# Kernel optimization log

Measured on AMD Instinct MI355X. Metric: run time of the kernel, lower is better.

## Reference

```python
import jax, jax.numpy as jnp
import numpy as np


def _gather_corner(flat_feats, iz, iy, ix, H, W, B, F, Hg, Wg):
    # flat_feats: [B, F, D*H*W]; iz/iy/ix: [B, Hg, Wg] int32 (already clamped)
    lin = (iz * H + iy) * W + ix                      # [B, Hg, Wg]
    lin = jnp.broadcast_to(lin.reshape(B, 1, Hg * Wg), (B, F, Hg * Wg))
    return jnp.take_along_axis(flat_feats, lin, axis=2).reshape(B, F, Hg, Wg)


def setup_inputs() -> dict:
    key = jax.random.key(0)
    k1, k2 = jax.random.split(key)
    input_feats = jax.random.normal(k1, (4, 8, 128, 128, 128), dtype=jnp.float32)
    sampling_grid = jax.random.normal(k2, (4, 512, 512, 3), dtype=jnp.float32)
    return {"input_feats": input_feats, "sampling_grid": sampling_grid}


def reference(input_feats, sampling_grid):
    B, F, D, H, W = input_feats.shape
    Hg, Wg = sampling_grid.shape[1], sampling_grid.shape[2]

    # map grid from [-1,1] to voxel coordinates [0, dim-1]
    g = jnp.clip(sampling_grid, -1.0, 1.0)
    scale = jnp.array([W - 1.0, H - 1.0, D - 1.0], dtype=sampling_grid.dtype)
    g = (g + 1.0) * 0.5 * scale                      # [B, Hg, Wg, 3] in x,y,z order
    x, y, z = g[..., 0], g[..., 1], g[..., 2]

    x0 = jnp.floor(x); y0 = jnp.floor(y); z0 = jnp.floor(z)
    u = (x - x0)[:, None]                            # [B,1,Hg,Wg]
    v = (y - y0)[:, None]
    w = (z - z0)[:, None]

    # nearest grid_sample with align_corners=True on integer coords == clamped index
    def clampi(a, hi):
        return jnp.clip(a, 0, hi).astype(jnp.int32)

    ix0 = clampi(x0, W - 1); ix1 = clampi(x0 + 1.0, W - 1)
    iy0 = clampi(y0, H - 1); iy1 = clampi(y0 + 1.0, H - 1)
    iz0 = clampi(z0, D - 1); iz1 = clampi(z0 + 1.0, D - 1)

    flat = input_feats.reshape(B, F, D * H * W)
    gc = lambda iz, iy, ix: _gather_corner(flat, iz, iy, ix, H, W, B, F, Hg, Wg)

    c000 = gc(iz0, iy0, ix0); c001 = gc(iz1, iy0, ix0)
    c010 = gc(iz0, iy1, ix0); c011 = gc(iz1, iy1, ix0)
    c100 = gc(iz0, iy0, ix1); c101 = gc(iz1, iy0, ix1)
    c110 = gc(iz0, iy1, ix1); c111 = gc(iz1, iy1, ix1)

    out = ((1 - u) * (1 - v) * (1 - w) * c000 + (1 - u) * (1 - v) * w * c001
           + (1 - u) * v * (1 - w) * c010 + (1 - u) * v * w * c011
           + u * (1 - v) * (1 - w) * c100 + u * (1 - v) * w * c101
           + u * v * (1 - w) * c110 + u * v * w * c111)
    return out  # [B, F, Hg, Wg]
```

## Files before the change

### kernel.cpp

```cpp
#include <hip/hip_runtime.h>
#include <hip/hip_fp16.h>


#define NB 4
#define NF 8
#define ND 128
#define NH 128
#define NW 128
#define HG 512
#define WG 512

typedef float        __attribute__((ext_vector_type(4))) f32x4;
typedef unsigned int __attribute__((ext_vector_type(4))) u32x4;

__global__ __launch_bounds__(256) void transform_kernel(
    const float* __restrict__ feats, __half* __restrict__ T)
{
    const size_t S = (size_t)ND * NH * NW;
    size_t tid = (size_t)blockIdx.x * blockDim.x + threadIdx.x;
    size_t b  = tid / (S / 4);
    size_t s4 = (tid - b * (S / 4)) * 4;

    const float* fb = feats + b * NF * S;
    __half* tb = T + (b * S + s4) * NF;

    f32x4 vals[NF];
#pragma unroll
    for (int f = 0; f < NF; ++f)
        vals[f] = __builtin_nontemporal_load(
            (const f32x4*)(fb + (size_t)f * S + s4));

#pragma unroll
    for (int i = 0; i < 4; ++i) {
        u32x4 hv;
#pragma unroll
        for (int f = 0; f < 4; ++f) {
            __half2 h = __floats2half2_rn(vals[2 * f][i], vals[2 * f + 1][i]);
            hv[f] = *(const unsigned*)&h;
        }
        *(u32x4*)(tb + (size_t)i * NF) = hv;
    }
}

__device__ __forceinline__ void pair_accum(
    const u32x4& lov, const u32x4& hiv, bool hi,
    float wr, float um, float u, float acc[NF])
{
    u32x4 c0 = hi ? hiv : lov;
    const u32x4& c1 = hiv;
#pragma unroll
    for (int j = 0; j < 4; ++j) {
        unsigned u0 = c0[j], u1 = c1[j];
        float2 f0 = __half22float2(*(const __half2*)&u0);
        float2 f1 = __half22float2(*(const __half2*)&u1);
        acc[2 * j]     = fmaf(wr, fmaf(u, f1.x, um * f0.x), acc[2 * j]);
        acc[2 * j + 1] = fmaf(wr, fmaf(u, f1.y, um * f0.y), acc[2 * j + 1]);
    }
}

__global__ __launch_bounds__(256) void trilerp_half_kernel(
    const __half* __restrict__ T,
    const float* __restrict__ grid,
    float* __restrict__ out)
{
    const int P = HG * WG;
    int idx = blockIdx.x * blockDim.x + threadIdx.x;
    int b = idx >> 18;
    int p = idx & (P - 1);

    const float* g = grid + (size_t)idx * 3;
    float x = __builtin_nontemporal_load(g + 0);
    float y = __builtin_nontemporal_load(g + 1);
    float z = __builtin_nontemporal_load(g + 2);

    x = fminf(fmaxf(x, -1.0f), 1.0f);
    y = fminf(fmaxf(y, -1.0f), 1.0f);
    z = fminf(fmaxf(z, -1.0f), 1.0f);
    x = (x + 1.0f) * 0.5f * (float)(NW - 1);
    y = (y + 1.0f) * 0.5f * (float)(NH - 1);
    z = (z + 1.0f) * 0.5f * (float)(ND - 1);

    float xf = floorf(x), yf = floorf(y), zf = floorf(z);
    float u = x - xf, v = y - yf, w = z - zf;
    float um = 1.0f - u, vm = 1.0f - v, wm = 1.0f - w;

    int ix0 = min(max((int)xf, 0), NW - 1);
    int iy0 = min(max((int)yf, 0), NH - 1);
    int iy1 = min(iy0 + 1, NH - 1);
    int iz0 = min(max((int)zf, 0), ND - 1);
    int iz1 = min(iz0 + 1, ND - 1);

    int xb = min(ix0, NW - 2);
    bool hi = (ix0 != xb);

    const __half* tb = T + (size_t)b * ((size_t)ND * NH * NW) * NF;
    size_t r00 = ((size_t)(iz0 * NH + iy0) * NW + xb) * NF;
    size_t r01 = ((size_t)(iz0 * NH + iy1) * NW + xb) * NF;
    size_t r10 = ((size_t)(iz1 * NH + iy0) * NW + xb) * NF;
    size_t r11 = ((size_t)(iz1 * NH + iy1) * NW + xb) * NF;

    u32x4 L[8];
    L[0] = *(const u32x4*)(tb + r00);
    L[1] = *(const u32x4*)(tb + r00 + NF);
    L[2] = *(const u32x4*)(tb + r01);
    L[3] = *(const u32x4*)(tb + r01 + NF);
    L[4] = *(const u32x4*)(tb + r10);
    L[5] = *(const u32x4*)(tb + r10 + NF);
    L[6] = *(const u32x4*)(tb + r11);
    L[7] = *(const u32x4*)(tb + r11 + NF);

    float acc[NF];
#pragma unroll
    for (int f = 0; f < NF; ++f) acc[f] = 0.0f;

    pair_accum(L[0], L[1], hi, wm * vm, um, u, acc);
    pair_accum(L[2], L[3], hi, wm * v,  um, u, acc);
    pair_accum(L[4], L[5], hi, w  * vm, um, u, acc);
    pair_accum(L[6], L[7], hi, w  * v,  um, u, acc);

    float* o = out + (size_t)b * NF * P + p;
#pragma unroll
    for (int f = 0; f < NF; ++f)
        __builtin_nontemporal_store(acc[f], o + (size_t)f * P);
}

__global__ __launch_bounds__(256) void trilerp_f32_kernel(
    const float* __restrict__ feats,
    const float* __restrict__ grid,
    float* __restrict__ out)
{
    const int P = HG * WG;
    int idx = blockIdx.x * blockDim.x + threadIdx.x;
    int b = idx >> 18;
    int p = idx & (P - 1);

    const float* g = grid + (size_t)idx * 3;
    float x = g[0], y = g[1], z = g[2];
    x = fminf(fmaxf(x, -1.0f), 1.0f);
    y = fminf(fmaxf(y, -1.0f), 1.0f);
    z = fminf(fmaxf(z, -1.0f), 1.0f);
    x = (x + 1.0f) * 0.5f * (float)(NW - 1);
    y = (y + 1.0f) * 0.5f * (float)(NH - 1);
    z = (z + 1.0f) * 0.5f * (float)(ND - 1);

    float xf = floorf(x), yf = floorf(y), zf = floorf(z);
    float u = x - xf, v = y - yf, w = z - zf;

    int ix0 = min(max((int)xf, 0), NW - 1);
    int ix1 = min(ix0 + 1, NW - 1);
    int iy0 = min(max((int)yf, 0), NH - 1);
    int iy1 = min(iy0 + 1, NH - 1);
    int iz0 = min(max((int)zf, 0), ND - 1);
    int iz1 = min(iz0 + 1, ND - 1);

    float um = 1.0f - u, vm = 1.0f - v, wm = 1.0f - w;
    float w000 = um * vm * wm, w100 = u * vm * wm;
    float w010 = um * v * wm,  w110 = u * v * wm;
    float w001 = um * vm * w,  w101 = u * vm * w;
    float w011 = um * v * w,   w111 = u * v * w;

    int off00 = (iz0 * NH + iy0) * NW;
    int off01 = (iz0 * NH + iy1) * NW;
    int off10 = (iz1 * NH + iy0) * NW;
    int off11 = (iz1 * NH + iy1) * NW;

    const size_t fstride = (size_t)ND * NH * NW;
    const float* fb = feats + (size_t)b * NF * fstride;
    float* o = out + (size_t)b * NF * P + p;

#pragma unroll
    for (int f = 0; f < NF; ++f) {
        const float* fp = fb + (size_t)f * fstride;
        float r = w000 * fp[off00 + ix0] + w100 * fp[off00 + ix1]
                + w010 * fp[off01 + ix0] + w110 * fp[off01 + ix1]
                + w001 * fp[off10 + ix0] + w101 * fp[off10 + ix1]
                + w011 * fp[off11 + ix0] + w111 * fp[off11 + ix1];
        o[(size_t)f * P] = r;
    }
}

extern "C" void kernel_launch(void* const* d_in, const int* in_sizes, int n_in,
                              void* d_out, int out_size, void* d_ws, size_t ws_size,
                              hipStream_t stream) {
    const float* feats = (const float*)d_in[0];
    const float* grid  = (const float*)d_in[1];
    float* out = (float*)d_out;

    const size_t needed = (size_t)NB * ND * NH * NW * NF * sizeof(__half);

    if (ws_size >= needed) {
        __half* T = (__half*)d_ws;
        const int tthreads = NB * ND * NH * NW / 4;
        transform_kernel<<<tthreads / 256, 256, 0, stream>>>(feats, T);
        const int total = NB * HG * WG;
        trilerp_half_kernel<<<total / 256, 256, 0, stream>>>(T, grid, out);
    } else {
        const int total = NB * HG * WG;
        trilerp_f32_kernel<<<total / 256, 256, 0, stream>>>(feats, grid, out);
    }
}
```

Before: 426.9 us.

## Bin samples by voxel region with counting sort before gathering for cache locality

Adds a counting-sort pipeline (histogram, single-block scan, atomic scatter) that groups grid samples into 8x8x8-voxel bins per batch. The half-precision trilinear gather then runs in sorted order, writing to a permuted buffer that a final kernel un-permutes into the output layout. The aim is to turn the random 8-corner gathers from the 128 MB fp16 volume into cache-friendly accesses. In exchange it adds five extra launches, atomics, a serial scan, and roughly 100 MB of extra payload, permuted-output and index traffic.

```diff
diff --git a/kernel.cpp b/kernel.cpp
--- a/kernel.cpp
+++ b/kernel.cpp
@@ -10,6 +10,10 @@
 #define HG 512
 #define WG 512
 
+#define PTOT (HG * WG)
+#define TOTAL (NB * PTOT)
+#define NBINS (NB * 16 * 16 * 16)
+
 typedef float        __attribute__((ext_vector_type(4))) f32x4;
 typedef unsigned int __attribute__((ext_vector_type(4))) u32x4;
 
@@ -40,6 +44,81 @@
         }
         *(u32x4*)(tb + (size_t)i * NF) = hv;
     }
+}
+
+__device__ __forceinline__ void grid_to_voxel(
+    const float* __restrict__ g, float& x, float& y, float& z)
+{
+    x = __builtin_nontemporal_load(g + 0);
+    y = __builtin_nontemporal_load(g + 1);
+    z = __builtin_nontemporal_load(g + 2);
+    x = fminf(fmaxf(x, -1.0f), 1.0f);
+    y = fminf(fmaxf(y, -1.0f), 1.0f);
+    z = fminf(fmaxf(z, -1.0f), 1.0f);
+    x = (x + 1.0f) * 0.5f * (float)(NW - 1);
+    y = (y + 1.0f) * 0.5f * (float)(NH - 1);
+    z = (z + 1.0f) * 0.5f * (float)(ND - 1);
+}
+
+__device__ __forceinline__ int sample_bin(int idx, float x, float y, float z)
+{
+    int ix0 = min(max((int)floorf(x), 0), NW - 1);
+    int iy0 = min(max((int)floorf(y), 0), NH - 1);
+    int iz0 = min(max((int)floorf(z), 0), ND - 1);
+    return ((((idx >> 18) * 16 + (iz0 >> 3)) * 16 + (iy0 >> 3)) * 16) + (ix0 >> 3);
+}
+
+__global__ __launch_bounds__(256) void zero_kernel(unsigned* __restrict__ hist)
+{
+    hist[blockIdx.x * blockDim.x + threadIdx.x] = 0u;
+}
+
+__global__ __launch_bounds__(256) void hist_kernel(
+    const float* __restrict__ grid, unsigned* __restrict__ hist)
+{
+    int idx = blockIdx.x * blockDim.x + threadIdx.x;
+    float x, y, z;
+    grid_to_voxel(grid + (size_t)idx * 3, x, y, z);
+    atomicAdd(&hist[sample_bin(idx, x, y, z)], 1u);
+}
+
+__global__ __launch_bounds__(1024) void scan_kernel(unsigned* __restrict__ hist)
+{
+    __shared__ unsigned part[1024];
+    int t = threadIdx.x;
+    unsigned v[16];
+    unsigned s = 0;
+#pragma unroll
+    for (int i = 0; i < 16; ++i) { v[i] = hist[t * 16 + i]; s += v[i]; }
+    part[t] = s;
+    __syncthreads();
+    for (int off = 1; off < 1024; off <<= 1) {
+        unsigned add = (t >= off) ? part[t - off] : 0u;
+        __syncthreads();
+        part[t] += add;
+        __syncthreads();
+    }
+    unsigned ex = (t == 0) ? 0u : part[t - 1];
+#pragma unroll
+    for (int i = 0; i < 16; ++i) { hist[t * 16 + i] = ex; ex += v[i]; }
+}
+
+__global__ __launch_bounds__(256) void scatter_kernel(
+    const float* __restrict__ grid, unsigned* __restrict__ cursor,
+    u32x4* __restrict__ payload, unsigned* __restrict__ invperm)
+{
+    int idx = blockIdx.x * blockDim.x + threadIdx.x;
+    float x, y, z;
+    grid_to_voxel(grid + (size_t)idx * 3, x, y, z);
+    int bin = sample_bin(idx, x, y, z);
+    unsigned slot = atomicAdd(&cursor[bin], 1u);
+    u32x4 pl;
+    pl.x = __float_as_uint(x);
+    pl.y = __float_as_uint(y);
+    pl.z = __float_as_uint(z);
+    pl.w = (unsigned)idx;
+    payload[slot] = pl;
+    invperm[idx] = slot;
 }
 
 __device__ __forceinline__ void pair_accum(
@@ -58,27 +137,16 @@
     }
 }
 
-__global__ __launch_bounds__(256) void trilerp_half_kernel(
-    const __half* __restrict__ T,
-    const float* __restrict__ grid,
-    float* __restrict__ out)
-{
-    const int P = HG * WG;
-    int idx = blockIdx.x * blockDim.x + threadIdx.x;
-    int b = idx >> 18;
-    int p = idx & (P - 1);
-
-    const float* g = grid + (size_t)idx * 3;
-    float x = __builtin_nontemporal_load(g + 0);
-    float y = __builtin_nontemporal_load(g + 1);
-    float z = __builtin_nontemporal_load(g + 2);
-
-    x = fminf(fmaxf(x, -1.0f), 1.0f);
-    y = fminf(fmaxf(y, -1.0f), 1.0f);
-    z = fminf(fmaxf(z, -1.0f), 1.0f);
-    x = (x + 1.0f) * 0.5f * (float)(NW - 1);
-    y = (y + 1.0f) * 0.5f * (float)(NH - 1);
-    z = (z + 1.0f) * 0.5f * (float)(ND - 1);
+__global__ __launch_bounds__(256) void gather_kernel(
+    const __half* __restrict__ T, const u32x4* __restrict__ payload,
+    float* __restrict__ outT)
+{
+    int slot = blockIdx.x * blockDim.x + threadIdx.x;
+    u32x4 pl = payload[slot];
+    float x = __uint_as_float(pl.x);
+    float y = __uint_as_float(pl.y);
+    float z = __uint_as_float(pl.z);
+    int b = (int)(pl.w >> 18);
 
     float xf = floorf(x), yf = floorf(y), zf = floorf(z);
     float u = x - xf, v = y - yf, w = z - zf;
@@ -118,6 +186,84 @@
     pair_accum(L[4], L[5], hi, w  * vm, um, u, acc);
     pair_accum(L[6], L[7], hi, w  * v,  um, u, acc);
 
+    f32x4* op = (f32x4*)(outT + (size_t)slot * NF);
+    f32x4 o0, o1;
+#pragma unroll
+    for (int j = 0; j < 4; ++j) { o0[j] = acc[j]; o1[j] = acc[4 + j]; }
+    op[0] = o0;
+    op[1] = o1;
+}
+
+__global__ __launch_bounds__(256) void unperm_kernel(
+    const float* __restrict__ outT, const unsigned* __restrict__ invperm,
+    float* __restrict__ out)
+{
+    int i = blockIdx.x * blockDim.x + threadIdx.x;
+    unsigned slot = invperm[i];
+    const f32x4* ip = (const f32x4*)(outT + (size_t)slot * NF);
+    f32x4 a = ip[0];
+    f32x4 c = ip[1];
+    int b = i >> 18;
+    int p = i & (PTOT - 1);
+    float* o = out + (size_t)b * NF * PTOT + p;
+#pragma unroll
+    for (int j = 0; j < 4; ++j) {
+        __builtin_nontemporal_store(a[j], o + (size_t)j * PTOT);
+        __builtin_nontemporal_store(c[j], o + (size_t)(4 + j) * PTOT);
+    }
+}
+
+__global__ __launch_bounds__(256) void trilerp_half_kernel(
+    const __half* __restrict__ T,
+    const float* __restrict__ grid,
+    float* __restrict__ out)
+{
+    const int P = HG * WG;
+    int idx = blockIdx.x * blockDim.x + threadIdx.x;
+    int b = idx >> 18;
+    int p = idx & (P - 1);
+
+    float x, y, z;
+    grid_to_voxel(grid + (size_t)idx * 3, x, y, z);
+
+    float xf = floorf(x), yf = floorf(y), zf = floorf(z);
+    float u = x - xf, v = y - yf, w = z - zf;
+    float um = 1.0f - u, vm = 1.0f - v, wm = 1.0f - w;
+
+    int ix0 = min(max((int)xf, 0), NW - 1);
+    int iy0 = min(max((int)yf, 0), NH - 1);
+    int iy1 = min(iy0 + 1, NH - 1);
+    int iz0 = min(max((int)zf, 0), ND - 1);
+    int iz1 = min(iz0 + 1, ND - 1);
+
+    int xb = min(ix0, NW - 2);
+    bool hi = (ix0 != xb);
+
+    const __half* tb = T + (size_t)b * ((size_t)ND * NH * NW) * NF;
+    size_t r00 = ((size_t)(iz0 * NH + iy0) * NW + xb) * NF;
+    size_t r01 = ((size_t)(iz0 * NH + iy1) * NW + xb) * NF;
+    size_t r10 = ((size_t)(iz1 * NH + iy0) * NW + xb) * NF;
+    size_t r11 = ((size_t)(iz1 * NH + iy1) * NW + xb) * NF;
+
+    u32x4 L[8];
+    L[0] = *(const u32x4*)(tb + r00);
+    L[1] = *(const u32x4*)(tb + r00 + NF);
+    L[2] = *(const u32x4*)(tb + r01);
+    L[3] = *(const u32x4*)(tb + r01 + NF);
+    L[4] = *(const u32x4*)(tb + r10);
+    L[5] = *(const u32x4*)(tb + r10 + NF);
+    L[6] = *(const u32x4*)(tb + r11);
+    L[7] = *(const u32x4*)(tb + r11 + NF);
+
+    float acc[NF];
+#pragma unroll
+    for (int f = 0; f < NF; ++f) acc[f] = 0.0f;
+
+    pair_accum(L[0], L[1], hi, wm * vm, um, u, acc);
+    pair_accum(L[2], L[3], hi, wm * v,  um, u, acc);
+    pair_accum(L[4], L[5], hi, w  * vm, um, u, acc);
+    pair_accum(L[6], L[7], hi, w  * v,  um, u, acc);
+
     float* o = out + (size_t)b * NF * P + p;
 #pragma unroll
     for (int f = 0; f < NF; ++f)
@@ -186,9 +332,31 @@
     const float* grid  = (const float*)d_in[1];
     float* out = (float*)d_out;
 
-    const size_t needed = (size_t)NB * ND * NH * NW * NF * sizeof(__half);
-
-    if (ws_size >= needed) {
+    const size_t T_BYTES    = (size_t)NB * ND * NH * NW * NF * sizeof(__half);
+    const size_t OFF_PAYL   = T_BYTES;
+    const size_t OFF_OUTT   = OFF_PAYL + (size_t)TOTAL * 16;
+    const size_t OFF_INVP   = OFF_OUTT + (size_t)TOTAL * NF * sizeof(float);
+    const size_t OFF_HIST   = OFF_INVP + (size_t)TOTAL * sizeof(unsigned);
+    const size_t NEED_FULL  = OFF_HIST + (size_t)NBINS * sizeof(unsigned);
+
+    if (ws_size >= NEED_FULL) {
+        char* ws = (char*)d_ws;
+        __half*   T       = (__half*)ws;
+        u32x4*    payload = (u32x4*)(ws + OFF_PAYL);
+        float*    outT    = (float*)(ws + OFF_OUTT);
+        unsigned* invperm = (unsigned*)(ws + OFF_INVP);
+        unsigned* hist    = (unsigned*)(ws + OFF_HIST);
+
+        const int tthreads = NB * ND * NH * NW / 4;
+        transform_kernel<<<tthreads / 256, 256, 0, stream>>>(feats, T);
+
+        zero_kernel<<<NBINS / 256, 256, 0, stream>>>(hist);
+        hist_kernel<<<TOTAL / 256, 256, 0, stream>>>(grid, hist);
+        scan_kernel<<<1, 1024, 0, stream>>>(hist);
+        scatter_kernel<<<TOTAL / 256, 256, 0, stream>>>(grid, hist, payload, invperm);
+        gather_kernel<<<TOTAL / 256, 256, 0, stream>>>(T, payload, outT);
+        unperm_kernel<<<TOTAL / 256, 256, 0, stream>>>(outT, invperm, out);
+    } else if (ws_size >= T_BYTES) {
         __half* T = (__half*)d_ws;
         const int tthreads = NB * ND * NH * NW / 4;
         transform_kernel<<<tthreads / 256, 256, 0, stream>>>(feats, T);
```

After: 757.5 us. 77.5% more time.
